# Kernel optimization log

Hardware: AMD Instinct MI355X
Metric: run time of the kernel (lower is better)

The kernel has to match this reference:

```python
import jax, jax.numpy as jnp
import numpy as np

B, NF, H = 1024, 64, 512


def setup_inputs() -> dict:
    key = jax.random.key(0)
    ks = jax.random.split(key, 12)
    sc_in2 = 1.0 / np.sqrt(2 * H)
    sc_in1 = 1.0 / np.sqrt(H)
    inp = {
        "field_vectors": jax.random.normal(ks[0], (B, NF, H), dtype=jnp.float32),
        # and_fusion: Linear(2H->H), ReLU, Linear(H->H)
        "and_W1": jax.random.uniform(ks[1], (2 * H, H), jnp.float32, -sc_in2, sc_in2),
        "and_b1": jax.random.uniform(ks[2], (H,), jnp.float32, -sc_in2, sc_in2),
        "and_W2": jax.random.uniform(ks[3], (H, H), jnp.float32, -sc_in1, sc_in1),
        "and_b2": jax.random.uniform(ks[4], (H,), jnp.float32, -sc_in1, sc_in1),
        # or_fusion: Linear(2H->H), ReLU, Linear(H->H)
        "or_W1": jax.random.uniform(ks[5], (2 * H, H), jnp.float32, -sc_in2, sc_in2),
        "or_b1": jax.random.uniform(ks[6], (H,), jnp.float32, -sc_in2, sc_in2),
        "or_W2": jax.random.uniform(ks[7], (H, H), jnp.float32, -sc_in1, sc_in1),
        "or_b2": jax.random.uniform(ks[8], (H,), jnp.float32, -sc_in1, sc_in1),
        # not_transform: Linear(H->H), Tanh
        "not_W": jax.random.uniform(ks[9], (H, H), jnp.float32, -sc_in1, sc_in1),
        "not_b": jax.random.uniform(ks[10], (H,), jnp.float32, -sc_in1, sc_in1),
        # Disjoint index structure so the torch skip-set logic is a no-op:
        # 'and' pairs use fields 0..31, 'or' pairs use 32..47, leftovers 48..63.
        "not_idx": 48 + jnp.arange(8, dtype=jnp.int32),
        "and_pairs": jnp.arange(32, dtype=jnp.int32).reshape(16, 2),
        "or_pairs": (32 + jnp.arange(16, dtype=jnp.int32)).reshape(8, 2),
        "leftover_idx": 48 + jnp.arange(16, dtype=jnp.int32),
    }
    return inp


def _mlp2(x, W1, b1, W2, b2):
    # Linear -> ReLU -> Linear
    return jax.nn.relu(x @ W1 + b1) @ W2 + b2


def reference(field_vectors, and_W1, and_b1, and_W2, and_b2,
              or_W1, or_b1, or_W2, or_b2, not_W, not_b,
              not_idx, and_pairs, or_pairs, leftover_idx):
    # In-place 'not' transform on selected fields (Tanh(Linear))
    fv = field_vectors.at[:, not_idx].set(
        jnp.tanh(field_vectors[:, not_idx] @ not_W + not_b))
    # Gather (i, j) pairs, concat along feature dim -> [B, P, 2H]
    cat_and = jnp.concatenate([fv[:, and_pairs[:, 0]], fv[:, and_pairs[:, 1]]], axis=-1)
    fused_and = _mlp2(cat_and, and_W1, and_b1, and_W2, and_b2)  # [B, 16, H]
    cat_or = jnp.concatenate([fv[:, or_pairs[:, 0]], fv[:, or_pairs[:, 1]]], axis=-1)
    fused_or = _mlp2(cat_or, or_W1, or_b1, or_W2, or_b2)  # [B, 8, H]
    # Stack order matches torch loop: and results, or results, untouched fields
    return jnp.concatenate([fused_and, fused_or, fv[:, leftover_idx]], axis=1)
```

## Files before the change

### kernel.cpp

```cpp
#include <hip/hip_runtime.h>
#include <hip/hip_bf16.h>
#include <math.h>

typedef __attribute__((ext_vector_type(8))) __bf16 bf16x8;
typedef __attribute__((ext_vector_type(4))) float f32x4;

__device__ __forceinline__ unsigned short f2bf(float f) {
    union { float f; unsigned u; } v; v.f = f;
    unsigned r = v.u + 0x7fffu + ((v.u >> 16) & 1u);
    return (unsigned short)(r >> 16);
}
__device__ __forceinline__ unsigned int pk(float a, float b) {
    union { float f; unsigned u; } x, y; x.f = a; y.f = b;
    unsigned ra = (x.u + 0x7fffu + ((x.u >> 16) & 1u)) >> 16;
    unsigned rb = (y.u + 0x7fffu + ((y.u >> 16) & 1u)) & 0xffff0000u;
    return ra | rb;
}

__device__ __forceinline__ void gl2lds16(const unsigned short* g, unsigned short* l) {
    __builtin_amdgcn_global_load_lds(
        (const __attribute__((address_space(1))) unsigned int*)(g),
        (__attribute__((address_space(3))) unsigned int*)(l), 16, 0, 0);
}

struct PrepArgs {
    const float* fv;
    unsigned short* fvb;
    const int *and_pairs, *or_pairs, *not_idx, *lidx;
    float* out;
    const float* W[5];
    unsigned short* WT[5];
    int K[5], N[5];
    int tstart[6];
};

__global__ __launch_bounds__(256) void prep_kernel(PrepArgs a) {
    __shared__ float tile[64][65];
    __shared__ int used[64];
    __shared__ int lslot[64];
    const int blk = blockIdx.x;
    const int tid = threadIdx.x;

    if (blk < 16384) {
        if (tid < 64) {
            const int f = tid;
            int u = 0;
            for (int i = 0; i < 32; i++) u |= (a.and_pairs[i] == f);
            for (int i = 0; i < 16; i++) u |= (a.or_pairs[i] == f);
            for (int i = 0; i < 8; i++)  u |= (a.not_idx[i] == f);
            used[f] = u;
            int ls = -1;
            for (int l = 0; l < 16; l++) if (a.lidx[l] == f) ls = l;
            lslot[f] = ls;
        }
        __syncthreads();

        const int t = blk * 256 + tid;
        const size_t e = (size_t)t * 8;
        const int c = (int)(e & 511);
        const int f = (int)((e >> 9) & 63);
        const int b = (int)(e >> 15);
        const int u = used[f], ls = lslot[f];
        if (u | (ls >= 0)) {
            const float4 v0 = *(const float4*)(a.fv + e);
            const float4 v1 = *(const float4*)(a.fv + e + 4);
            if (u) {
                uint4 o;
                o.x = pk(v0.x, v0.y); o.y = pk(v0.z, v0.w);
                o.z = pk(v1.x, v1.y); o.w = pk(v1.z, v1.w);
                ((uint4*)a.fvb)[t] = o;
            }
            if (ls >= 0) {
                float* d = a.out + ((size_t)b * 40 + 24 + ls) * 512 + c;
                *(float4*)(d)     = v0;
                *(float4*)(d + 4) = v1;
            }
        }
    } else {
        const int bx = blk - 16384;
        int m = 0;
        while (bx >= a.tstart[m + 1]) m++;
        const float* src = a.W[m];
        unsigned short* dst = a.WT[m];
        const int K = a.K[m], N = a.N[m];
        const int t = bx - a.tstart[m];
        const int ntn = N >> 6;
        const int tk = t / ntn, tn = t % ntn;
        const int c = tid & 63, r0 = tid >> 6;
        #pragma unroll
        for (int r = r0; r < 64; r += 4)
            tile[r][c] = src[(size_t)(tk * 64 + r) * N + tn * 64 + c];
        __syncthreads();
        #pragma unroll
        for (int r = r0; r < 64; r += 4)
            dst[(size_t)(tn * 64 + r) * K + tk * 64 + c] = f2bf(tile[c][r]);
    }
}

template <int P, int K, int SRCM, int EPIM, int QBASE>
__device__ __forceinline__ void gemm_seg(
    const unsigned short* __restrict__ A,
    const int* __restrict__ idx,
    const unsigned short* __restrict__ WT,
    const float* __restrict__ bias,
    unsigned short* __restrict__ hid_out,
    float* __restrict__ out,
    const int* __restrict__ leftover,
    int local,
    unsigned short* As, unsigned short* Bs) {

    const int tid  = threadIdx.x;
    const int lane = tid & 63, w = tid >> 6;
    const int tm = (local >> 2) * 128, tn = (local & 3) * 128;

    const int lm  = lane >> 2;
    const int kin = (((lane & 3) ^ ((lane >> 2) & 3)) * 8);
    const unsigned short* ar0[2];
    const unsigned short* ar1[2];
    const unsigned short* wp[2];
    #pragma unroll
    for (int c = 0; c < 2; c++) {
        const int m = tm + w * 32 + c * 16 + lm;
        if constexpr (SRCM == 0) {
            const int b = m / P, p = m % P;
            ar0[c] = A + ((size_t)b * 64 + idx[2 * p]) * 512;
            ar1[c] = A + ((size_t)b * 64 + idx[2 * p + 1]) * 512;
        } else if constexpr (SRCM == 1) {
            const int b = m >> 3, i = m & 7;
            ar0[c] = A + ((size_t)b * 64 + idx[i]) * 512;
        } else {
            ar0[c] = A + (size_t)m * K;
        }
        const int n = tn + w * 32 + c * 16 + lm;
        wp[c] = WT + (size_t)n * K;
    }

    f32x4 acc[4][4];
    #pragma unroll
    for (int i = 0; i < 4; i++)
        #pragma unroll
        for (int j = 0; j < 4; j++)
            acc[i][j] = f32x4{0.f, 0.f, 0.f, 0.f};

    const int wm = (w & 1) * 64, wn = (w >> 1) * 64;
    const int xsel = ((lane >> 4) ^ (lane & 3)) * 8;

    for (int k0 = 0; k0 < K; k0 += 32) {
        __syncthreads();
        #pragma unroll
        for (int c = 0; c < 2; c++) {
            const unsigned short* asrc;
            if constexpr (SRCM == 0)
                asrc = (k0 >= 512 ? ar1[c] + (k0 - 512) : ar0[c] + k0) + kin;
            else
                asrc = ar0[c] + k0 + kin;
            gl2lds16(asrc, &As[w * 1024 + c * 512]);
            gl2lds16(wp[c] + k0 + kin, &Bs[w * 1024 + c * 512]);
        }
        __syncthreads();

        bf16x8 af[4], bfr[4];
        #pragma unroll
        for (int mi = 0; mi < 4; mi++)
            af[mi] = *(const bf16x8*)&As[(wm + mi * 16 + (lane & 15)) * 32 + xsel];
        #pragma unroll
        for (int ni = 0; ni < 4; ni++)
            bfr[ni] = *(const bf16x8*)&Bs[(wn + ni * 16 + (lane & 15)) * 32 + xsel];
        #pragma unroll
        for (int mi = 0; mi < 4; mi++)
            #pragma unroll
            for (int ni = 0; ni < 4; ni++)
                acc[mi][ni] = __builtin_amdgcn_mfma_f32_16x16x32_bf16(
                    af[mi], bfr[ni], acc[mi][ni], 0, 0, 0);
    }

    const int col0 = tn + wn + (lane & 15);
    const int row0 = tm + wm + (lane >> 4) * 4;

    int qmap[8];
    if constexpr (EPIM == 2) {
        #pragma unroll
        for (int i = 0; i < 8; i++) {
            const int f = idx[i];
            int q = 24;
            for (int l = 0; l < 16; l++)
                if (leftover[l] == f) q = 24 + l;
            qmap[i] = q;
        }
    }

    #pragma unroll
    for (int ni = 0; ni < 4; ni++) {
        const int n  = col0 + ni * 16;
        const float bv = bias[n];
        #pragma unroll
        for (int mi = 0; mi < 4; mi++) {
            const int rbase = row0 + mi * 16;
            #pragma unroll
            for (int j = 0; j < 4; j++) {
                const int m = rbase + j;
                float v = acc[mi][ni][j] + bv;
                if constexpr (EPIM == 0) {
                    v = v > 0.f ? v : 0.f;
                    hid_out[(size_t)m * 512 + n] = f2bf(v);
                } else if constexpr (EPIM == 1) {
                    const int b = m / P, p = m % P;
                    out[((size_t)b * 40 + QBASE + p) * 512 + n] = v;
                } else {
                    const int b = m >> 3, i = m & 7;
                    out[((size_t)b * 40 + qmap[i]) * 512 + n] = tanhf(v);
                }
            }
        }
    }
}

struct L1Args {
    const unsigned short *fvb, *and_W1T, *or_W1T, *not_WT;
    const int *and_pairs, *or_pairs, *not_idx, *leftover;
    const float *and_b1, *or_b1, *not_b;
    unsigned short *and_hid, *or_hid;
    float* out;
};

__global__ __launch_bounds__(256, 3) void l1_phase(L1Args a) {
    __shared__ __align__(16) unsigned short As[128 * 32];
    __shared__ __align__(16) unsigned short Bs[128 * 32];
    const int blk = blockIdx.x;
    if (blk < 512)
        gemm_seg<16, 1024, 0, 0, 0>(a.fvb, a.and_pairs, a.and_W1T, a.and_b1,
                                    a.and_hid, nullptr, nullptr, blk, As, Bs);
    else if (blk < 768)
        gemm_seg<8, 1024, 0, 0, 0>(a.fvb, a.or_pairs, a.or_W1T, a.or_b1,
                                   a.or_hid, nullptr, nullptr, blk - 512, As, Bs);
    else
        gemm_seg<8, 512, 1, 2, 24>(a.fvb, a.not_idx, a.not_WT, a.not_b,
                                   nullptr, a.out, a.leftover, blk - 768, As, Bs);
}

struct L2Args {
    const unsigned short *and_hid, *or_hid, *and_W2T, *or_W2T;
    const float *and_b2, *or_b2;
    float* out;
};

__global__ __launch_bounds__(256, 3) void l2_phase(L2Args a) {
    __shared__ __align__(16) unsigned short As[128 * 32];
    __shared__ __align__(16) unsigned short Bs[128 * 32];
    const int blk = blockIdx.x;
    if (blk < 512)
        gemm_seg<16, 512, 2, 1, 0>(a.and_hid, nullptr, a.and_W2T, a.and_b2,
                                   nullptr, a.out, nullptr, blk, As, Bs);
    else
        gemm_seg<8, 512, 2, 1, 16>(a.or_hid, nullptr, a.or_W2T, a.or_b2,
                                   nullptr, a.out, nullptr, blk - 512, As, Bs);
}

extern "C" void kernel_launch(void* const* d_in, const int* in_sizes, int n_in,
                              void* d_out, int out_size, void* d_ws, size_t ws_size,
                              hipStream_t stream) {
    const float* fv       = (const float*)d_in[0];
    const float* and_W1   = (const float*)d_in[1];
    const float* and_b1   = (const float*)d_in[2];
    const float* and_W2   = (const float*)d_in[3];
    const float* and_b2   = (const float*)d_in[4];
    const float* or_W1    = (const float*)d_in[5];
    const float* or_b1    = (const float*)d_in[6];
    const float* or_W2    = (const float*)d_in[7];
    const float* or_b2    = (const float*)d_in[8];
    const float* not_W    = (const float*)d_in[9];
    const float* not_b    = (const float*)d_in[10];
    const int* not_idx    = (const int*)d_in[11];
    const int* and_pairs  = (const int*)d_in[12];
    const int* or_pairs   = (const int*)d_in[13];
    const int* leftover   = (const int*)d_in[14];
    float* out = (float*)d_out;
    char* ws = (char*)d_ws;

    unsigned short* fvb     = (unsigned short*)(ws);
    unsigned short* and_W1T = (unsigned short*)(ws + 67108864);
    unsigned short* or_W1T  = (unsigned short*)(ws + 68157440);
    unsigned short* and_W2T = (unsigned short*)(ws + 69206016);
    unsigned short* or_W2T  = (unsigned short*)(ws + 69730304);
    unsigned short* not_WT  = (unsigned short*)(ws + 70254592);
    unsigned short* and_hid = (unsigned short*)(ws + 70778880);
    unsigned short* or_hid  = (unsigned short*)(ws + 87556096);

    PrepArgs pa;
    pa.fv = fv; pa.fvb = fvb; pa.out = out;
    pa.and_pairs = and_pairs; pa.or_pairs = or_pairs;
    pa.not_idx = not_idx; pa.lidx = leftover;
    pa.W[0] = and_W1; pa.WT[0] = and_W1T; pa.K[0] = 1024; pa.N[0] = 512;
    pa.W[1] = or_W1;  pa.WT[1] = or_W1T;  pa.K[1] = 1024; pa.N[1] = 512;
    pa.W[2] = and_W2; pa.WT[2] = and_W2T; pa.K[2] = 512;  pa.N[2] = 512;
    pa.W[3] = or_W2;  pa.WT[3] = or_W2T;  pa.K[3] = 512;  pa.N[3] = 512;
    pa.W[4] = not_W;  pa.WT[4] = not_WT;  pa.K[4] = 512;  pa.N[4] = 512;
    pa.tstart[0] = 0;   pa.tstart[1] = 128; pa.tstart[2] = 256;
    pa.tstart[3] = 320; pa.tstart[4] = 384; pa.tstart[5] = 448;
    prep_kernel<<<dim3(16832), dim3(256), 0, stream>>>(pa);

    L1Args g1;
    g1.fvb = fvb; g1.and_W1T = and_W1T; g1.or_W1T = or_W1T; g1.not_WT = not_WT;
    g1.and_pairs = and_pairs; g1.or_pairs = or_pairs; g1.not_idx = not_idx;
    g1.leftover = leftover;
    g1.and_b1 = and_b1; g1.or_b1 = or_b1; g1.not_b = not_b;
    g1.and_hid = and_hid; g1.or_hid = or_hid; g1.out = out;
    l1_phase<<<dim3(1024), dim3(256), 0, stream>>>(g1);

    L2Args g2;
    g2.and_hid = and_hid; g2.or_hid = or_hid;
    g2.and_W2T = and_W2T; g2.or_W2T = or_W2T;
    g2.and_b2 = and_b2; g2.or_b2 = or_b2; g2.out = out;
    l2_phase<<<dim3(768), dim3(256), 0, stream>>>(g2);
}
```

Before: 344.1 us.

## Double-buffer GEMM LDS tiles and split field-table setup from bf16 conversion

The GEMM main loop now uses two LDS buffers, issuing the global-to-LDS load for the next K-slice before computing on the current one, with one barrier per iteration instead of two. A separate setup kernel builds a per-field table (used flag and leftover slot) and transposes the weights. The conversion kernel then reads that table instead of every block recomputing the flags. There is a subtle change: fields in not_idx no longer get their leftover copy written, and the conversion kernel now reads fv unconditionally, even for unused fields. Doubled LDS use may reduce occupancy.

Result: no change. 338.9 us (-1.5%).

```diff
diff --git a/kernel.cpp b/kernel.cpp
--- a/kernel.cpp
+++ b/kernel.cpp
@@ -23,77 +23,83 @@
         (__attribute__((address_space(3))) unsigned int*)(l), 16, 0, 0);
 }
 
-struct PrepArgs {
-    const float* fv;
-    unsigned short* fvb;
+struct SetupArgs {
     const int *and_pairs, *or_pairs, *not_idx, *lidx;
-    float* out;
+    int* tbl;
     const float* W[5];
     unsigned short* WT[5];
     int K[5], N[5];
     int tstart[6];
 };
 
-__global__ __launch_bounds__(256) void prep_kernel(PrepArgs a) {
+__global__ __launch_bounds__(256) void setup_kernel(SetupArgs a) {
     __shared__ float tile[64][65];
-    __shared__ int used[64];
-    __shared__ int lslot[64];
     const int blk = blockIdx.x;
     const int tid = threadIdx.x;
 
-    if (blk < 16384) {
+    if (blk == 0) {
         if (tid < 64) {
             const int f = tid;
             int u = 0;
             for (int i = 0; i < 32; i++) u |= (a.and_pairs[i] == f);
             for (int i = 0; i < 16; i++) u |= (a.or_pairs[i] == f);
-            for (int i = 0; i < 8; i++)  u |= (a.not_idx[i] == f);
-            used[f] = u;
+            int isnot = 0;
+            for (int i = 0; i < 8; i++)  isnot |= (a.not_idx[i] == f);
             int ls = -1;
             for (int l = 0; l < 16; l++) if (a.lidx[l] == f) ls = l;
-            lslot[f] = ls;
-        }
-        __syncthreads();
-
-        const int t = blk * 256 + tid;
-        const size_t e = (size_t)t * 8;
-        const int c = (int)(e & 511);
-        const int f = (int)((e >> 9) & 63);
-        const int b = (int)(e >> 15);
-        const int u = used[f], ls = lslot[f];
-        if (u | (ls >= 0)) {
-            const float4 v0 = *(const float4*)(a.fv + e);
-            const float4 v1 = *(const float4*)(a.fv + e + 4);
-            if (u) {
-                uint4 o;
-                o.x = pk(v0.x, v0.y); o.y = pk(v0.z, v0.w);
-                o.z = pk(v1.x, v1.y); o.w = pk(v1.z, v1.w);
-                ((uint4*)a.fvb)[t] = o;
-            }
-            if (ls >= 0) {
-                float* d = a.out + ((size_t)b * 40 + 24 + ls) * 512 + c;
-                *(float4*)(d)     = v0;
-                *(float4*)(d + 4) = v1;
-            }
-        }
-    } else {
-        const int bx = blk - 16384;
-        int m = 0;
-        while (bx >= a.tstart[m + 1]) m++;
-        const float* src = a.W[m];
-        unsigned short* dst = a.WT[m];
-        const int K = a.K[m], N = a.N[m];
-        const int t = bx - a.tstart[m];
-        const int ntn = N >> 6;
-        const int tk = t / ntn, tn = t % ntn;
-        const int c = tid & 63, r0 = tid >> 6;
-        #pragma unroll
-        for (int r = r0; r < 64; r += 4)
-            tile[r][c] = src[(size_t)(tk * 64 + r) * N + tn * 64 + c];
-        __syncthreads();
-        #pragma unroll
-        for (int r = r0; r < 64; r += 4)
-            dst[(size_t)(tn * 64 + r) * K + tk * 64 + c] = f2bf(tile[c][r]);
+            if (isnot) ls = -1;
+            a.tbl[f] = (u | isnot) | ((ls + 1) << 8);
+        }
+        return;
+    }
+
+    const int bx = blk - 1;
+    int m = 0;
+    while (bx >= a.tstart[m + 1]) m++;
+    const float* src = a.W[m];
+    unsigned short* dst = a.WT[m];
+    const int K = a.K[m], N = a.N[m];
+    const int t = bx - a.tstart[m];
+    const int ntn = N >> 6;
+    const int tk = t / ntn, tn = t % ntn;
+    const int c = tid & 63, r0 = tid >> 6;
+    #pragma unroll
+    for (int r = r0; r < 64; r += 4)
+        tile[r][c] = src[(size_t)(tk * 64 + r) * N + tn * 64 + c];
+    __syncthreads();
+    #pragma unroll
+    for (int r = r0; r < 64; r += 4)
+        dst[(size_t)(tn * 64 + r) * K + tk * 64 + c] = f2bf(tile[c][r]);
+}
+
+struct PrepArgs {
+    const float* fv;
+    unsigned short* fvb;
+    const int* tbl;
+    float* out;
+};
+
+__global__ __launch_bounds__(256) void prep_kernel(PrepArgs a) {
+    const int t = blockIdx.x * 256 + threadIdx.x;
+    const size_t e = (size_t)t * 8;
+    const int c = (int)(e & 511);
+    const int f = (int)((e >> 9) & 63);
+    const int b = (int)(e >> 15);
+    const float4 v0 = *(const float4*)(a.fv + e);
+    const float4 v1 = *(const float4*)(a.fv + e + 4);
+    const int tb = a.tbl[f];
+    const int u  = tb & 0xff;
+    const int ls = (tb >> 8) - 1;
+    if (u) {
+        uint4 o;
+        o.x = pk(v0.x, v0.y); o.y = pk(v0.z, v0.w);
+        o.z = pk(v1.x, v1.y); o.w = pk(v1.z, v1.w);
+        ((uint4*)a.fvb)[t] = o;
+    }
+    if (ls >= 0) {
+        float* d = a.out + ((size_t)b * 40 + 24 + ls) * 512 + c;
+        *(float4*)(d)     = v0;
+        *(float4*)(d + 4) = v1;
     }
 }
 
@@ -145,8 +151,7 @@
     const int wm = (w & 1) * 64, wn = (w >> 1) * 64;
     const int xsel = ((lane >> 4) ^ (lane & 3)) * 8;
 
-    for (int k0 = 0; k0 < K; k0 += 32) {
-        __syncthreads();
+    auto stage = [&](int buf, int k0) {
         #pragma unroll
         for (int c = 0; c < 2; c++) {
             const unsigned short* asrc;
@@ -154,24 +159,34 @@
                 asrc = (k0 >= 512 ? ar1[c] + (k0 - 512) : ar0[c] + k0) + kin;
             else
                 asrc = ar0[c] + k0 + kin;
-            gl2lds16(asrc, &As[w * 1024 + c * 512]);
-            gl2lds16(wp[c] + k0 + kin, &Bs[w * 1024 + c * 512]);
-        }
-        __syncthreads();
-
+            gl2lds16(asrc, &As[buf * 4096 + w * 1024 + c * 512]);
+            gl2lds16(wp[c] + k0 + kin, &Bs[buf * 4096 + w * 1024 + c * 512]);
+        }
+    };
+
+    constexpr int NT = K / 32;
+    stage(0, 0);
+    __syncthreads();
+
+    for (int t = 0; t < NT; t++) {
+        const int cur = t & 1;
+        if (t + 1 < NT) stage(cur ^ 1, (t + 1) * 32);
+        const unsigned short* Ab = &As[cur * 4096];
+        const unsigned short* Bb = &Bs[cur * 4096];
         bf16x8 af[4], bfr[4];
         #pragma unroll
         for (int mi = 0; mi < 4; mi++)
-            af[mi] = *(const bf16x8*)&As[(wm + mi * 16 + (lane & 15)) * 32 + xsel];
+            af[mi] = *(const bf16x8*)&Ab[(wm + mi * 16 + (lane & 15)) * 32 + xsel];
         #pragma unroll
         for (int ni = 0; ni < 4; ni++)
-            bfr[ni] = *(const bf16x8*)&Bs[(wn + ni * 16 + (lane & 15)) * 32 + xsel];
+            bfr[ni] = *(const bf16x8*)&Bb[(wn + ni * 16 + (lane & 15)) * 32 + xsel];
         #pragma unroll
         for (int mi = 0; mi < 4; mi++)
             #pragma unroll
             for (int ni = 0; ni < 4; ni++)
                 acc[mi][ni] = __builtin_amdgcn_mfma_f32_16x16x32_bf16(
                     af[mi], bfr[ni], acc[mi][ni], 0, 0, 0);
+        __syncthreads();
     }
 
     const int col0 = tn + wn + (lane & 15);
@@ -224,8 +239,8 @@
 };
 
 __global__ __launch_bounds__(256, 3) void l1_phase(L1Args a) {
-    __shared__ __align__(16) unsigned short As[128 * 32];
-    __shared__ __align__(16) unsigned short Bs[128 * 32];
+    __shared__ __align__(16) unsigned short As[2 * 128 * 32];
+    __shared__ __align__(16) unsigned short Bs[2 * 128 * 32];
     const int blk = blockIdx.x;
     if (blk < 512)
         gemm_seg<16, 1024, 0, 0, 0>(a.fvb, a.and_pairs, a.and_W1T, a.and_b1,
@@ -245,8 +260,8 @@
 };
 
 __global__ __launch_bounds__(256, 3) void l2_phase(L2Args a) {
-    __shared__ __align__(16) unsigned short As[128 * 32];
-    __shared__ __align__(16) unsigned short Bs[128 * 32];
+    __shared__ __align__(16) unsigned short As[2 * 128 * 32];
+    __shared__ __align__(16) unsigned short Bs[2 * 128 * 32];
     const int blk = blockIdx.x;
     if (blk < 512)
         gemm_seg<16, 512, 2, 1, 0>(a.and_hid, nullptr, a.and_W2T, a.and_b2,
@@ -285,19 +300,23 @@
     unsigned short* not_WT  = (unsigned short*)(ws + 70254592);
     unsigned short* and_hid = (unsigned short*)(ws + 70778880);
     unsigned short* or_hid  = (unsigned short*)(ws + 87556096);
+    int*            tbl     = (int*)(ws + 95944704);
+
+    SetupArgs sa;
+    sa.and_pairs = and_pairs; sa.or_pairs = or_pairs;
+    sa.not_idx = not_idx; sa.lidx = leftover; sa.tbl = tbl;
+    sa.W[0] = and_W1; sa.WT[0] = and_W1T; sa.K[0] = 1024; sa.N[0] = 512;
+    sa.W[1] = or_W1;  sa.WT[1] = or_W1T;  sa.K[1] = 1024; sa.N[1] = 512;
+    sa.W[2] = and_W2; sa.WT[2] = and_W2T; sa.K[2] = 512;  sa.N[2] = 512;
+    sa.W[3] = or_W2;  sa.WT[3] = or_W2T;  sa.K[3] = 512;  sa.N[3] = 512;
+    sa.W[4] = not_W;  sa.WT[4] = not_WT;  sa.K[4] = 512;  sa.N[4] = 512;
+    sa.tstart[0] = 0;   sa.tstart[1] = 128; sa.tstart[2] = 256;
+    sa.tstart[3] = 320; sa.tstart[4] = 384; sa.tstart[5] = 448;
+    setup_kernel<<<dim3(449), dim3(256), 0, stream>>>(sa);
 
     PrepArgs pa;
-    pa.fv = fv; pa.fvb = fvb; pa.out = out;
-    pa.and_pairs = and_pairs; pa.or_pairs = or_pairs;
-    pa.not_idx = not_idx; pa.lidx = leftover;
-    pa.W[0] = and_W1; pa.WT[0] = and_W1T; pa.K[0] = 1024; pa.N[0] = 512;
-    pa.W[1] = or_W1;  pa.WT[1] = or_W1T;  pa.K[1] = 1024; pa.N[1] = 512;
-    pa.W[2] = and_W2; pa.WT[2] = and_W2T; pa.K[2] = 512;  pa.N[2] = 512;
-    pa.W[3] = or_W2;  pa.WT[3] = or_W2T;  pa.K[3] = 512;  pa.N[3] = 512;
-    pa.W[4] = not_W;  pa.WT[4] = not_WT;  pa.K[4] = 512;  pa.N[4] = 512;
-    pa.tstart[0] = 0;   pa.tstart[1] = 128; pa.tstart[2] = 256;
-    pa.tstart[3] = 320; pa.tstart[4] = 384; pa.tstart[5] = 448;
-    prep_kernel<<<dim3(16832), dim3(256), 0, stream>>>(pa);
+    pa.fv = fv; pa.fvb = fvb; pa.tbl = tbl; pa.out = out;
+    prep_kernel<<<dim3(16384), dim3(256), 0, stream>>>(pa);
 
     L1Args g1;
     g1.fvb = fvb; g1.and_W1T = and_W1T; g1.or_W1T = or_W1T; g1.not_WT = not_WT;
```
